# Kernel optimization log

Measured on AMD Instinct MI355X. Metric: run time of the kernel, lower is better.

Reference implementation:

```python
import jax, jax.numpy as jnp
import numpy as np

DECAY = 0.99
EPS = 1e-5
NUM_EMBEDDINGS = 8192


def setup_inputs() -> dict:
    key = jax.random.key(0)
    k1, k2 = jax.random.split(key)
    N, D, K = 65536, 64, NUM_EMBEDDINGS
    x = jax.random.normal(k1, (N, D), dtype=jnp.float32)
    vq_embedding = jax.random.uniform(k2, (K, D), dtype=jnp.float32)
    vq_cluster_size = jnp.ones((K,), dtype=jnp.float32)
    return {"x": x, "vq_embedding": vq_embedding, "vq_cluster_size": vq_cluster_size}


def reference(x, vq_embedding, vq_cluster_size):
    N, D = x.shape
    K = vq_embedding.shape[0]

    # BatchNorm1d(affine=False), training mode: normalize with batch stats (biased var)
    mean = jnp.mean(x, axis=0)                      # [D]
    var = jnp.var(x, axis=0)                        # biased, [D]
    xn = (x - mean) / jnp.sqrt(var + EPS)           # [N, D]

    # pairwise squared distances [N, K]
    distances = (jnp.sum(xn * xn, axis=1, keepdims=True)
                 + jnp.sum(vq_embedding * vq_embedding, axis=1)
                 - 2.0 * (xn @ vq_embedding.T))
    idx = jnp.argmin(distances, axis=1)             # [N]

    # one-hot scatter expressed as segment sums
    dw = jax.ops.segment_sum(xn, idx, num_segments=K)                      # [K, D]
    counts = jax.ops.segment_sum(jnp.ones((N,), x.dtype), idx, num_segments=K)  # [K]

    # EMA codebook update
    new_emb = vq_cluster_size[:, None] * vq_embedding * DECAY + (1.0 - DECAY) * dw
    new_size = vq_cluster_size * DECAY + (1.0 - DECAY) * counts
    new_emb = new_emb / new_size[:, None]

    # BN running stats with momentum=None (cumulative avg, first batch):
    # running_mean = batch mean, running_var = unbiased batch var
    unbiased_var = var * (N / (N - 1))
    running_std = jnp.sqrt(unbiased_var + EPS)
    vq_embedding_output = new_emb * running_std[None, :] + mean[None, :]

    return vq_embedding_output, new_emb, new_size
```

## Files before the change

kernel.cpp:

```cpp
#include <hip/hip_runtime.h>

#define NROWS 65536
#define DIM 64
#define KCODES 8192
#define DECAYF 0.99f
#define EPSV 1e-5f
#define KD (KCODES * DIM)
#define KSPLIT 4
#define KC (KCODES / KSPLIT)
#define ROUNDS (KC / 128)

typedef _Float16 half8 __attribute__((ext_vector_type(8)));
typedef float f32x16 __attribute__((ext_vector_type(16)));

#define WS_STATS  0
#define WS_NHCK   256
#define WS_EBUF   8448
#define WS_PSUM   270592
#define WS_PSQ    286976
#define WS_PACKED 303360
#define WS_DW     368896
#define WS_COUNTS 893184

__global__ __launch_bounds__(256) void k_colstats_partial(
    const float* __restrict__ x, float* __restrict__ psum, float* __restrict__ psq)
{
    const int wave = threadIdx.x >> 6;
    const int col  = threadIdx.x & 63;
    const int base = blockIdx.x * 256;
    float s = 0.f, q = 0.f;
    #pragma unroll 4
    for (int i = 0; i < 64; ++i) {
        int r = base + i * 4 + wave;
        float v = x[(size_t)r * DIM + col];
        s += v;
        q += v * v;
    }
    __shared__ float ls[4][64];
    __shared__ float lq[4][64];
    ls[wave][col] = s;
    lq[wave][col] = q;
    __syncthreads();
    if (threadIdx.x < 64) {
        psum[blockIdx.x * 64 + col] = ls[0][col] + ls[1][col] + ls[2][col] + ls[3][col];
        psq[blockIdx.x * 64 + col]  = lq[0][col] + lq[1][col] + lq[2][col] + lq[3][col];
    }
}

__global__ void k_colstats_final(const float* __restrict__ psum,
                                 const float* __restrict__ psq,
                                 float* __restrict__ stats)
{
    const int col = threadIdx.x;
    float s = 0.f, q = 0.f;
    for (int i = 0; i < 256; ++i) {
        s += psum[i * 64 + col];
        q += psq[i * 64 + col];
    }
    const float n = (float)NROWS;
    float mean = s / n;
    float var = q / n - mean * mean;
    if (var < 0.f) var = 0.f;
    stats[col]       = mean;
    stats[64 + col]  = 1.0f / sqrtf(var + EPSV);
    stats[128 + col] = sqrtf(var * (n / (n - 1.0f)) + EPSV);
}

__global__ __launch_bounds__(256) void k_prep(const float* __restrict__ emb,
                                              half8* __restrict__ ebuf,
                                              float* __restrict__ nhck)
{
    const int tid = blockIdx.x * 256 + threadIdx.x;
    const int code = tid >> 3, sub = tid & 7;
    const int c = sub >> 1, h = sub & 1;
    const int d0 = c * 16 + h * 8;
    const float* e = emb + (size_t)code * DIM + d0;
    float4 a = *(const float4*)e;
    float4 b = *(const float4*)(e + 4);
    float f[8] = {a.x, a.y, a.z, a.w, b.x, b.y, b.z, b.w};
    half8 hh;
    float ssq = 0.f;
    #pragma unroll
    for (int i = 0; i < 8; ++i) {
        hh[i] = (_Float16)(f[i] - 0.5f);
        ssq += f[i] * f[i];
    }
    #pragma unroll
    for (int o = 1; o < 8; o <<= 1) ssq += __shfl_xor(ssq, o, 64);
    if (sub == 0) nhck[code] = 10.6875f - 0.5f * ssq;
    const int R = code >> 7, t = (code >> 5) & 3, col = code & 31;
    ebuf[(size_t)R * 1024 + t * 256 + c * 64 + h * 32 + col] = hh;
}

__device__ __forceinline__ void gload16(const void* g, void* l)
{
    __builtin_amdgcn_global_load_lds(
        (const __attribute__((address_space(1))) void*)g,
        (__attribute__((address_space(3))) void*)l, 16, 0, 0);
}

__global__ __launch_bounds__(256) void k_argmin32(
    const float* __restrict__ x, const half8* __restrict__ ebuf,
    const float* __restrict__ nhckg, const float* __restrict__ stats,
    unsigned* __restrict__ packed)
{
    __shared__ half8 smem[2048];

    const int lane = threadIdx.x & 63;
    const int wave = threadIdx.x >> 6;
    const int kc = blockIdx.y;
    const int col = lane & 31, h = lane >> 5;
    const int myrow = blockIdx.x * 128 + wave * 32 + col;

    half8 ah[4];
    {
        const float* xr = x + (size_t)myrow * DIM + h * 8;
        #pragma unroll
        for (int c = 0; c < 4; ++c) {
            float4 v0  = *(const float4*)(xr + c * 16);
            float4 v1  = *(const float4*)(xr + c * 16 + 4);
            float4 mu0 = *(const float4*)(stats + h * 8 + c * 16);
            float4 mu1 = *(const float4*)(stats + h * 8 + c * 16 + 4);
            float4 sg0 = *(const float4*)(stats + 64 + h * 8 + c * 16);
            float4 sg1 = *(const float4*)(stats + 64 + h * 8 + c * 16 + 4);
            ah[c][0] = (_Float16)((v0.x - mu0.x) * sg0.x);
            ah[c][1] = (_Float16)((v0.y - mu0.y) * sg0.y);
            ah[c][2] = (_Float16)((v0.z - mu0.z) * sg0.z);
            ah[c][3] = (_Float16)((v0.w - mu0.w) * sg0.w);
            ah[c][4] = (_Float16)((v1.x - mu1.x) * sg1.x);
            ah[c][5] = (_Float16)((v1.y - mu1.y) * sg1.y);
            ah[c][6] = (_Float16)((v1.z - mu1.z) * sg1.z);
            ah[c][7] = (_Float16)((v1.w - mu1.w) * sg1.w);
        }
    }

    float best[16];
    #pragma unroll
    for (int i = 0; i < 16; ++i) best[i] = -3.4e38f;

    const half8* esrc = ebuf + (size_t)kc * (KC * 8);
    const float* ckb = nhckg + kc * KC;

    {
        const char* src = (const char*)esrc + threadIdx.x * 16;
        char* dst = (char*)smem + threadIdx.x * 16;
        #pragma unroll
        for (int i = 0; i < 4; ++i) gload16(src + i * 4096, dst + i * 4096);
    }
    float nhck[4];
    #pragma unroll
    for (int t = 0; t < 4; ++t) nhck[t] = ckb[t * 32 + col];
    __syncthreads();

    for (int R = 0; R < ROUNDS; ++R) {
        const int buf = R & 1;
        float nhck_n[4] = {0.f, 0.f, 0.f, 0.f};
        if (R < ROUNDS - 1) {
            const char* src = (const char*)esrc + (size_t)(R + 1) * 16384 + threadIdx.x * 16;
            char* dst = (char*)smem + (buf ^ 1) * 16384 + threadIdx.x * 16;
            #pragma unroll
            for (int i = 0; i < 4; ++i) gload16(src + i * 4096, dst + i * 4096);
            #pragma unroll
            for (int t = 0; t < 4; ++t) nhck_n[t] = ckb[(R + 1) * 128 + t * 32 + col];
        }

        const half8* sb = smem + buf * 1024 + lane;
        #pragma unroll
        for (int t = 0; t < 4; ++t) {
            half8 b0 = sb[t * 256];
            half8 b1 = sb[t * 256 + 64];
            half8 b2 = sb[t * 256 + 128];
            half8 b3 = sb[t * 256 + 192];
            f32x16 acc;
            #pragma unroll
            for (int i = 0; i < 16; ++i) acc[i] = nhck[t];
            __builtin_amdgcn_s_setprio(1);
            acc = __builtin_amdgcn_mfma_f32_32x32x16_f16(ah[0], b0, acc, 0, 0, 0);
            acc = __builtin_amdgcn_mfma_f32_32x32x16_f16(ah[1], b1, acc, 0, 0, 0);
            acc = __builtin_amdgcn_mfma_f32_32x32x16_f16(ah[2], b2, acc, 0, 0, 0);
            acc = __builtin_amdgcn_mfma_f32_32x32x16_f16(ah[3], b3, acc, 0, 0, 0);
            __builtin_amdgcn_s_setprio(0);
            const unsigned key = (unsigned)(8191 - (kc * KC + R * 128 + t * 32 + col));
            #pragma unroll
            for (int i = 0; i < 16; ++i) {
                unsigned u = (__float_as_uint(acc[i]) & 0xFFFFE000u) | key;
                best[i] = fmaxf(best[i], __uint_as_float(u));
            }
        }
        __syncthreads();
        #pragma unroll
        for (int t = 0; t < 4; ++t) nhck[t] = nhck_n[t];
    }

    #pragma unroll
    for (int off = 1; off < 32; off <<= 1) {
        #pragma unroll
        for (int i = 0; i < 16; ++i)
            best[i] = fmaxf(best[i], __shfl_xor(best[i], off, 64));
    }
    if (col == 0) {
        const int rbase = blockIdx.x * 128 + wave * 32 + 4 * h;
        #pragma unroll
        for (int i = 0; i < 16; ++i) {
            int row = rbase + (i & 3) + 8 * (i >> 2);
            unsigned u = __float_as_uint(best[i]);
            u = (u & 0x80000000u) ? ~u : (u | 0x80000000u);
            atomicMax(&packed[row], u);
        }
    }
}

__global__ __launch_bounds__(256) void k_scatter(
    const float* __restrict__ x, const float* __restrict__ stats,
    const unsigned* __restrict__ packed,
    float* __restrict__ dw, float* __restrict__ counts)
{
    const int t = blockIdx.x * 256 + threadIdx.x;
    const int row = t >> 6, col = t & 63;
    const unsigned v = packed[row];
    const unsigned key = (v & 0x80000000u) ? (v & 8191u) : (~v & 8191u);
    const int j = 8191 - (int)key;
    float xv = (x[(size_t)row * DIM + col] - stats[col]) * stats[64 + col];
    atomicAdd(&dw[(size_t)j * DIM + col], xv);
    if (col == 0) atomicAdd(&counts[j], 1.0f);
}

__global__ __launch_bounds__(256) void k_final(
    const float* __restrict__ emb, const float* __restrict__ cs,
    const float* __restrict__ dw, const float* __restrict__ counts,
    const float* __restrict__ stats, float* __restrict__ out)
{
    const int t = blockIdx.x * 256 + threadIdx.x;
    const int k = t >> 6, d = t & 63;
    float csk = cs[k];
    float ns = csk * DECAYF + (1.f - DECAYF) * counts[k];
    float ne = (csk * emb[t] * DECAYF + (1.f - DECAYF) * dw[t]) / ns;
    out[KD + t] = ne;
    out[t] = ne * stats[128 + d] + stats[d];
    if (d == 0) out[2 * KD + k] = ns;
}

extern "C" void kernel_launch(void* const* d_in, const int* in_sizes, int n_in,
                              void* d_out, int out_size, void* d_ws, size_t ws_size,
                              hipStream_t stream)
{
    const float* x   = (const float*)d_in[0];
    const float* emb = (const float*)d_in[1];
    const float* cs  = (const float*)d_in[2];
    float* out = (float*)d_out;
    float* ws  = (float*)d_ws;

    float* stats  = ws + WS_STATS;
    float* nhck   = ws + WS_NHCK;
    half8* ebuf   = (half8*)(ws + WS_EBUF);
    float* psum   = ws + WS_PSUM;
    float* psq    = ws + WS_PSQ;
    unsigned* packed = (unsigned*)(ws + WS_PACKED);
    float* dw     = ws + WS_DW;
    float* counts = ws + WS_COUNTS;

    hipMemsetAsync(ws + WS_PACKED, 0,
                   (size_t)(65536 + KD + KCODES) * sizeof(float), stream);

    k_colstats_partial<<<256, 256, 0, stream>>>(x, psum, psq);
    k_colstats_final<<<1, 64, 0, stream>>>(psum, psq, stats);
    k_prep<<<256, 256, 0, stream>>>(emb, ebuf, nhck);
    dim3 g3(NROWS / 128, KSPLIT);
    k_argmin32<<<g3, 256, 0, stream>>>(x, ebuf, nhck, stats, packed);
    k_scatter<<<(NROWS * DIM) / 256, 256, 0, stream>>>(x, stats, packed, dw, counts);
    k_final<<<KD / 256, 256, 0, stream>>>(emb, cs, dw, counts, stats, out);
}
```

Measured before the change: 157.9 us.

## Load codebook tiles directly from global memory instead of LDS double-buffering

The argmin kernel no longer stages codebook tiles into shared memory with async global-to-LDS loads, double buffering and per-round barriers. Each wave now reads its half8 B fragments and norm terms straight from global memory (served from L2/L1), one 32-code tile per iteration with unroll 2. The codebook layout is flattened to match. This removes the LDS traffic, the LDS allocation and the block-wide syncs, and may raise occupancy. In exchange, each wave issues its own global loads, so latency hiding depends on the cache hit rate and on the small unroll.

```diff
diff --git a/kernel.cpp b/kernel.cpp
--- a/kernel.cpp
+++ b/kernel.cpp
@@ -8,7 +8,7 @@
 #define KD (KCODES * DIM)
 #define KSPLIT 4
 #define KC (KCODES / KSPLIT)
-#define ROUNDS (KC / 128)
+#define NTILES (KC / 32)
 
 typedef _Float16 half8 __attribute__((ext_vector_type(8)));
 typedef float f32x16 __attribute__((ext_vector_type(16)));
@@ -88,15 +88,8 @@
     #pragma unroll
     for (int o = 1; o < 8; o <<= 1) ssq += __shfl_xor(ssq, o, 64);
     if (sub == 0) nhck[code] = 10.6875f - 0.5f * ssq;
-    const int R = code >> 7, t = (code >> 5) & 3, col = code & 31;
-    ebuf[(size_t)R * 1024 + t * 256 + c * 64 + h * 32 + col] = hh;
-}
-
-__device__ __forceinline__ void gload16(const void* g, void* l)
-{
-    __builtin_amdgcn_global_load_lds(
-        (const __attribute__((address_space(1))) void*)g,
-        (__attribute__((address_space(3))) void*)l, 16, 0, 0);
+    const int T = code >> 5, col = code & 31;
+    ebuf[(size_t)T * 256 + c * 64 + h * 32 + col] = hh;
 }
 
 __global__ __launch_bounds__(256) void k_argmin32(
@@ -104,8 +97,6 @@
     const float* __restrict__ nhckg, const float* __restrict__ stats,
     unsigned* __restrict__ packed)
 {
-    __shared__ half8 smem[2048];
-
     const int lane = threadIdx.x & 63;
     const int wave = threadIdx.x >> 6;
     const int kc = blockIdx.y;
@@ -138,58 +129,33 @@
     #pragma unroll
     for (int i = 0; i < 16; ++i) best[i] = -3.4e38f;
 
-    const half8* esrc = ebuf + (size_t)kc * (KC * 8);
-    const float* ckb = nhckg + kc * KC;
-
-    {
-        const char* src = (const char*)esrc + threadIdx.x * 16;
-        char* dst = (char*)smem + threadIdx.x * 16;
-        #pragma unroll
-        for (int i = 0; i < 4; ++i) gload16(src + i * 4096, dst + i * 4096);
-    }
-    float nhck[4];
-    #pragma unroll
-    for (int t = 0; t < 4; ++t) nhck[t] = ckb[t * 32 + col];
-    __syncthreads();
-
-    for (int R = 0; R < ROUNDS; ++R) {
-        const int buf = R & 1;
-        float nhck_n[4] = {0.f, 0.f, 0.f, 0.f};
-        if (R < ROUNDS - 1) {
-            const char* src = (const char*)esrc + (size_t)(R + 1) * 16384 + threadIdx.x * 16;
-            char* dst = (char*)smem + (buf ^ 1) * 16384 + threadIdx.x * 16;
-            #pragma unroll
-            for (int i = 0; i < 4; ++i) gload16(src + i * 4096, dst + i * 4096);
-            #pragma unroll
-            for (int t = 0; t < 4; ++t) nhck_n[t] = ckb[(R + 1) * 128 + t * 32 + col];
+    const half8* esrc = ebuf + (size_t)kc * (KC * 8) + h * 32 + col;
+    const float* ckb = nhckg + kc * KC + col;
+    const unsigned kbase = (unsigned)(8191 - kc * KC - col);
+
+    #pragma unroll 2
+    for (int T = 0; T < NTILES; ++T) {
+        const half8* p = esrc + T * 256;
+        half8 b0 = p[0];
+        half8 b1 = p[64];
+        half8 b2 = p[128];
+        half8 b3 = p[192];
+        float nv = ckb[T * 32];
+        const unsigned key = kbase - (unsigned)(T * 32);
+        f32x16 acc;
+        #pragma unroll
+        for (int i = 0; i < 16; ++i) acc[i] = nv;
+        __builtin_amdgcn_s_setprio(1);
+        acc = __builtin_amdgcn_mfma_f32_32x32x16_f16(ah[0], b0, acc, 0, 0, 0);
+        acc = __builtin_amdgcn_mfma_f32_32x32x16_f16(ah[1], b1, acc, 0, 0, 0);
+        acc = __builtin_amdgcn_mfma_f32_32x32x16_f16(ah[2], b2, acc, 0, 0, 0);
+        acc = __builtin_amdgcn_mfma_f32_32x32x16_f16(ah[3], b3, acc, 0, 0, 0);
+        __builtin_amdgcn_s_setprio(0);
+        #pragma unroll
+        for (int i = 0; i < 16; ++i) {
+            unsigned u = (__float_as_uint(acc[i]) & 0xFFFFE000u) | key;
+            best[i] = fmaxf(best[i], __uint_as_float(u));
         }
-
-        const half8* sb = smem + buf * 1024 + lane;
-        #pragma unroll
-        for (int t = 0; t < 4; ++t) {
-            half8 b0 = sb[t * 256];
-            half8 b1 = sb[t * 256 + 64];
-            half8 b2 = sb[t * 256 + 128];
-            half8 b3 = sb[t * 256 + 192];
-            f32x16 acc;
-            #pragma unroll
-            for (int i = 0; i < 16; ++i) acc[i] = nhck[t];
-            __builtin_amdgcn_s_setprio(1);
-            acc = __builtin_amdgcn_mfma_f32_32x32x16_f16(ah[0], b0, acc, 0, 0, 0);
-            acc = __builtin_amdgcn_mfma_f32_32x32x16_f16(ah[1], b1, acc, 0, 0, 0);
-            acc = __builtin_amdgcn_mfma_f32_32x32x16_f16(ah[2], b2, acc, 0, 0, 0);
-            acc = __builtin_amdgcn_mfma_f32_32x32x16_f16(ah[3], b3, acc, 0, 0, 0);
-            __builtin_amdgcn_s_setprio(0);
-            const unsigned key = (unsigned)(8191 - (kc * KC + R * 128 + t * 32 + col));
-            #pragma unroll
-            for (int i = 0; i < 16; ++i) {
-                unsigned u = (__float_as_uint(acc[i]) & 0xFFFFE000u) | key;
-                best[i] = fmaxf(best[i], __uint_as_float(u));
-            }
-        }
-        __syncthreads();
-        #pragma unroll
-        for (int t = 0; t < 4; ++t) nhck[t] = nhck_n[t];
     }
 
     #pragma unroll
```

New measurement: 169.4 us. 1.07x slower.

## Fuse memset, codebook prep, and column stats into one kernel; parallelize stats final

Applied to the files above, without the earlier changes.

Merges the workspace zeroing memset, the codebook fp16 conversion, and the partial column-stats pass into a single kernel launch. It also widens the final stats reduction from 64 to 256 threads, with a shared-memory combine at the end. This cuts two launches plus a memset from the front of the pipeline and shortens a serial reduction. The argmin key is also masked to 13 bits, which has no effect for valid indices.

```diff
diff --git a/kernel.cpp b/kernel.cpp
--- a/kernel.cpp
+++ b/kernel.cpp
@@ -21,75 +21,93 @@
 #define WS_PACKED 303360
 #define WS_DW     368896
 #define WS_COUNTS 893184
-
-__global__ __launch_bounds__(256) void k_colstats_partial(
-    const float* __restrict__ x, float* __restrict__ psum, float* __restrict__ psq)
-{
-    const int wave = threadIdx.x >> 6;
-    const int col  = threadIdx.x & 63;
-    const int base = blockIdx.x * 256;
+#define ZERO_F4   149504
+
+__global__ __launch_bounds__(256) void k_prep_stats(
+    const float* __restrict__ emb, const float* __restrict__ x,
+    half8* __restrict__ ebuf, float* __restrict__ nhck,
+    float* __restrict__ psum, float* __restrict__ psq,
+    float4* __restrict__ zbase)
+{
+    const int tid = blockIdx.x * 256 + threadIdx.x;
+
+    #pragma unroll
+    for (int i = 0; i < 3; ++i) {
+        int z = tid + i * 65536;
+        if (z < ZERO_F4) zbase[z] = float4{0.f, 0.f, 0.f, 0.f};
+    }
+
+    {
+        const int code = tid >> 3, sub = tid & 7;
+        const int c = sub >> 1, h = sub & 1;
+        const float* e = emb + (size_t)code * DIM + c * 16 + h * 8;
+        float4 a = *(const float4*)e;
+        float4 b = *(const float4*)(e + 4);
+        float f[8] = {a.x, a.y, a.z, a.w, b.x, b.y, b.z, b.w};
+        half8 hh;
+        float ssq = 0.f;
+        #pragma unroll
+        for (int i = 0; i < 8; ++i) {
+            hh[i] = (_Float16)(f[i] - 0.5f);
+            ssq += f[i] * f[i];
+        }
+        #pragma unroll
+        for (int o = 1; o < 8; o <<= 1) ssq += __shfl_xor(ssq, o, 64);
+        if (sub == 0) nhck[code] = 10.6875f - 0.5f * ssq;
+        const int R = code >> 7, t = (code >> 5) & 3, col = code & 31;
+        ebuf[(size_t)R * 1024 + t * 256 + c * 64 + h * 32 + col] = hh;
+    }
+
+    {
+        const int wave = threadIdx.x >> 6;
+        const int col  = threadIdx.x & 63;
+        const int base = blockIdx.x * 256;
+        float s = 0.f, q = 0.f;
+        #pragma unroll 4
+        for (int i = 0; i < 64; ++i) {
+            int r = base + i * 4 + wave;
+            float v = x[(size_t)r * DIM + col];
+            s += v;
+            q += v * v;
+        }
+        __shared__ float ls[4][64];
+        __shared__ float lq[4][64];
+        ls[wave][col] = s;
+        lq[wave][col] = q;
+        __syncthreads();
+        if (threadIdx.x < 64) {
+            psum[blockIdx.x * 64 + col] = ls[0][col] + ls[1][col] + ls[2][col] + ls[3][col];
+            psq[blockIdx.x * 64 + col]  = lq[0][col] + lq[1][col] + lq[2][col] + lq[3][col];
+        }
+    }
+}
+
+__global__ __launch_bounds__(256) void k_colstats_final(
+    const float* __restrict__ psum, const float* __restrict__ psq,
+    float* __restrict__ stats)
+{
+    const int col = threadIdx.x & 63, part = threadIdx.x >> 6;
     float s = 0.f, q = 0.f;
-    #pragma unroll 4
-    for (int i = 0; i < 64; ++i) {
-        int r = base + i * 4 + wave;
-        float v = x[(size_t)r * DIM + col];
-        s += v;
-        q += v * v;
+    for (int i = part * 64; i < part * 64 + 64; ++i) {
+        s += psum[i * 64 + col];
+        q += psq[i * 64 + col];
     }
     __shared__ float ls[4][64];
     __shared__ float lq[4][64];
-    ls[wave][col] = s;
-    lq[wave][col] = q;
+    ls[part][col] = s;
+    lq[part][col] = q;
     __syncthreads();
     if (threadIdx.x < 64) {
-        psum[blockIdx.x * 64 + col] = ls[0][col] + ls[1][col] + ls[2][col] + ls[3][col];
-        psq[blockIdx.x * 64 + col]  = lq[0][col] + lq[1][col] + lq[2][col] + lq[3][col];
-    }
-}
-
-__global__ void k_colstats_final(const float* __restrict__ psum,
-                                 const float* __restrict__ psq,
-                                 float* __restrict__ stats)
-{
-    const int col = threadIdx.x;
-    float s = 0.f, q = 0.f;
-    for (int i = 0; i < 256; ++i) {
-        s += psum[i * 64 + col];
-        q += psq[i * 64 + col];
-    }
-    const float n = (float)NROWS;
-    float mean = s / n;
-    float var = q / n - mean * mean;
-    if (var < 0.f) var = 0.f;
-    stats[col]       = mean;
-    stats[64 + col]  = 1.0f / sqrtf(var + EPSV);
-    stats[128 + col] = sqrtf(var * (n / (n - 1.0f)) + EPSV);
-}
-
-__global__ __launch_bounds__(256) void k_prep(const float* __restrict__ emb,
-                                              half8* __restrict__ ebuf,
-                                              float* __restrict__ nhck)
-{
-    const int tid = blockIdx.x * 256 + threadIdx.x;
-    const int code = tid >> 3, sub = tid & 7;
-    const int c = sub >> 1, h = sub & 1;
-    const int d0 = c * 16 + h * 8;
-    const float* e = emb + (size_t)code * DIM + d0;
-    float4 a = *(const float4*)e;
-    float4 b = *(const float4*)(e + 4);
-    float f[8] = {a.x, a.y, a.z, a.w, b.x, b.y, b.z, b.w};
-    half8 hh;
-    float ssq = 0.f;
-    #pragma unroll
-    for (int i = 0; i < 8; ++i) {
-        hh[i] = (_Float16)(f[i] - 0.5f);
-        ssq += f[i] * f[i];
-    }
-    #pragma unroll
-    for (int o = 1; o < 8; o <<= 1) ssq += __shfl_xor(ssq, o, 64);
-    if (sub == 0) nhck[code] = 10.6875f - 0.5f * ssq;
-    const int R = code >> 7, t = (code >> 5) & 3, col = code & 31;
-    ebuf[(size_t)R * 1024 + t * 256 + c * 64 + h * 32 + col] = hh;
+        s = ls[0][col] + ls[1][col] + ls[2][col] + ls[3][col];
+        q = lq[0][col] + lq[1][col] + lq[2][col] + lq[3][col];
+        const float n = (float)NROWS;
+        float mean = s / n;
+        float var = q / n - mean * mean;
+        if (var < 0.f) var = 0.f;
+        stats[col]       = mean;
+        stats[64 + col]  = 1.0f / sqrtf(var + EPSV);
+        stats[128 + col] = sqrtf(var * (n / (n - 1.0f)) + EPSV);
+    }
 }
 
 __device__ __forceinline__ void gload16(const void* g, void* l)
@@ -180,7 +198,8 @@
             acc = __builtin_amdgcn_mfma_f32_32x32x16_f16(ah[2], b2, acc, 0, 0, 0);
             acc = __builtin_amdgcn_mfma_f32_32x32x16_f16(ah[3], b3, acc, 0, 0, 0);
             __builtin_amdgcn_s_setprio(0);
-            const unsigned key = (unsigned)(8191 - (kc * KC + R * 128 + t * 32 + col));
+            const unsigned key =
+                (unsigned)(8191 - (kc * KC + R * 128 + t * 32 + col)) & 0x1FFFu;
             #pragma unroll
             for (int i = 0; i < 16; ++i) {
                 unsigned u = (__float_as_uint(acc[i]) & 0xFFFFE000u) | key;
@@ -259,12 +278,9 @@
     float* dw     = ws + WS_DW;
     float* counts = ws + WS_COUNTS;
 
-    hipMemsetAsync(ws + WS_PACKED, 0,
-                   (size_t)(65536 + KD + KCODES) * sizeof(float), stream);
-
-    k_colstats_partial<<<256, 256, 0, stream>>>(x, psum, psq);
-    k_colstats_final<<<1, 64, 0, stream>>>(psum, psq, stats);
-    k_prep<<<256, 256, 0, stream>>>(emb, ebuf, nhck);
+    k_prep_stats<<<256, 256, 0, stream>>>(emb, x, ebuf, nhck, psum, psq,
+                                          (float4*)(ws + WS_PACKED));
+    k_colstats_final<<<1, 256, 0, stream>>>(psum, psq, stats);
     dim3 g3(NROWS / 128, KSPLIT);
     k_argmin32<<<g3, 256, 0, stream>>>(x, ebuf, nhck, stats, packed);
     k_scatter<<<(NROWS * DIM) / 256, 256, 0, stream>>>(x, stats, packed, dw, counts);
```

Result: slower. 175.2 us (+11.0%).
